# Performance work log

Measured on AMD Instinct MI355X. Metric: run time of the kernel, lower is better.

Reference implementation:

```python
import jax, jax.numpy as jnp
import numpy as np

B, C, H, W = 4, 256, 64, 64
E = C // 8  # embedding_channels = inChannels // k


def setup_inputs() -> dict:
    key = jax.random.key(0)
    ks = jax.random.split(key, 9)
    sc = 1.0 / np.sqrt(C)
    so = 1.0 / np.sqrt(E)
    return {
        "x": jax.random.normal(ks[0], (B, C, H, W), dtype=jnp.float32),
        "Wk": jax.random.normal(ks[1], (E, C), dtype=jnp.float32) * sc,
        "bk": jax.random.normal(ks[2], (E,), dtype=jnp.float32) * 0.01,
        "Wq": jax.random.normal(ks[3], (E, C), dtype=jnp.float32) * sc,
        "bq": jax.random.normal(ks[4], (E,), dtype=jnp.float32) * 0.01,
        "Wv": jax.random.normal(ks[5], (E, C), dtype=jnp.float32) * sc,
        "bv": jax.random.normal(ks[6], (E,), dtype=jnp.float32) * 0.01,
        "Wo": jax.random.normal(ks[7], (C, E), dtype=jnp.float32) * so,
        "bo": jax.random.normal(ks[8], (C,), dtype=jnp.float32) * 0.01,
    }


def reference(x, Wk, bk, Wq, bq, Wv, bv, Wo, bo):
    b, c, h, w = x.shape
    n = h * w
    gamma = jnp.float32(0.5)  # non-learned branch (learned=False default)

    def conv1x1(inp, Wt, bt):
        # 1x1 conv == channel-mixing matmul: [b,c,h,w] x [e,c] -> [b,e,h,w]
        return jnp.einsum('bchw,ec->behw', inp, Wt) + bt[None, :, None, None]

    f = conv1x1(x, Wk, bk).reshape(b, -1, n)  # key   [b,E,N]
    g = conv1x1(x, Wq, bq).reshape(b, -1, n)  # query [b,E,N]
    hx = conv1x1(x, Wv, bv).reshape(b, -1, n)  # value [b,E,N]

    s = jnp.einsum('bei,bej->bij', f, g)       # f^T @ g, [b,N,N]
    beta = jax.nn.softmax(s, axis=1)           # softmax over dim 1 (rows) as in torch
    v = jnp.einsum('bei,bij->bej', hx, beta)   # h @ beta, [b,E,N]
    v = v.reshape(b, -1, h, w)

    o = jnp.einsum('behw,ce->bchw', v, Wo) + bo[None, :, None, None]
    y = gamma * o + x
    return y, o, gamma
```

## Files before the change

kernel.cpp:

```cpp
#include <hip/hip_runtime.h>

#define B_ 4
#define C_ 256
#define N_ 4096
#define E_ 32

typedef _Float16 f16x8 __attribute__((ext_vector_type(8)));
typedef _Float16 f16x4 __attribute__((ext_vector_type(4)));
typedef _Float16 f16x2 __attribute__((ext_vector_type(2)));
typedef float f32x4 __attribute__((ext_vector_type(4)));

#define LOG2E 1.44269504088896f
#define EXP2(x) __builtin_amdgcn_exp2f(x)
#define PKRTZ(a, b) __builtin_bit_cast(f16x2, __builtin_amdgcn_cvt_pkrtz((a), (b)))

#define XSWZ(row, col) ((col) ^ ((((row) >> 2) & 7) << 3))

__global__ __launch_bounds__(256) void proj_kernel(
    const float* __restrict__ x,
    const float* __restrict__ Wk, const float* __restrict__ bk,
    const float* __restrict__ Wq, const float* __restrict__ bq,
    const float* __restrict__ Wv, const float* __restrict__ bv,
    const float* __restrict__ Wo,
    _Float16* __restrict__ Qb, _Float16* __restrict__ Kb, _Float16* __restrict__ Vt,
    _Float16* __restrict__ Wof16, float* __restrict__ out)
{
    const int b  = blockIdx.x >> 7;
    const int n0 = (blockIdx.x & 127) << 5;
    const int t    = threadIdx.x;
    const int lane = t & 63;
    const int wave = t >> 6;
    const int l15  = lane & 15;
    const int quad = lane >> 4;

    if (blockIdx.x < 256 && t < 8) {
        float4 wv = ((const float4*)(Wo + blockIdx.x * E_))[t];
        f16x4 tp = {(_Float16)wv.x, (_Float16)wv.y, (_Float16)wv.z, (_Float16)wv.w};
        *(f16x4*)&Wof16[blockIdx.x * E_ + t * 4] = tp;
    }
    if (blockIdx.x == 0 && t == 0)
        out[(size_t)2 * B_ * C_ * N_] = 0.5f;

    __shared__ _Float16 xT[32][264];
    __shared__ _Float16 Wl[32][264];
    __shared__ _Float16 vT[32][44];

    for (int i4 = t; i4 < (32 * 256) / 4; i4 += 256) {
        int j4 = (i4 & 7) * 4;
        int c  = i4 >> 3;
        float4 xv = *(const float4*)(x + (size_t)(b * C_ + c) * N_ + n0 + j4);
        xT[j4 + 0][XSWZ(j4 + 0, c)] = (_Float16)xv.x;
        xT[j4 + 1][XSWZ(j4 + 1, c)] = (_Float16)xv.y;
        xT[j4 + 2][XSWZ(j4 + 2, c)] = (_Float16)xv.z;
        xT[j4 + 3][XSWZ(j4 + 3, c)] = (_Float16)xv.w;
    }

    const float* Ws[3] = {Wk, Wq, Wv};
    const float* bs[3] = {bk, bq, bv};

    const int rowg = wave >> 1;
    const int et   = wave & 1;
    const int row  = rowg * 16 + l15;
    f16x8 Bf[8];

    for (int m = 0; m < 3; ++m) {
        for (int i4 = t; i4 < (E_ * C_) / 4; i4 += 256) {
            float4 wv = ((const float4*)Ws[m])[i4];
            int e = (i4 * 4) >> 8, c = (i4 * 4) & 255;
            f16x4 tp = {(_Float16)wv.x, (_Float16)wv.y, (_Float16)wv.z, (_Float16)wv.w};
            *(f16x4*)&Wl[e][XSWZ(e, c)] = tp;
        }
        __syncthreads();
        if (m == 0) {
            #pragma unroll
            for (int kk = 0; kk < 8; ++kk)
                Bf[kk] = *(const f16x8*)&xT[row][XSWZ(row, kk * 32 + quad * 8)];
        }
        const float sc = (m == 1) ? LOG2E : 1.0f;
        const float* bias = bs[m];
        f32x4 acc = {0.f, 0.f, 0.f, 0.f};
        #pragma unroll
        for (int kk = 0; kk < 8; ++kk) {
            const int e = et * 16 + l15;
            f16x8 Af = *(const f16x8*)&Wl[e][XSWZ(e, kk * 32 + quad * 8)];
            acc = __builtin_amdgcn_mfma_f32_16x16x32_f16(Af, Bf[kk], acc, 0, 0, 0);
        }
        const int n  = n0 + row;
        const int e0 = et * 16 + quad * 4;
        if (m == 2) {
            #pragma unroll
            for (int r = 0; r < 4; ++r)
                vT[e0 + r][row] = (_Float16)(acc[r] + bias[e0 + r]);
        } else {
            f16x4 st;
            #pragma unroll
            for (int r = 0; r < 4; ++r)
                st[r] = (_Float16)((acc[r] + bias[e0 + r]) * sc);
            _Float16* dst = (m == 0) ? Kb : Qb;
            *(f16x4*)&dst[(size_t)(b * N_ + n) * E_ + e0] = st;
        }
        __syncthreads();
    }

    if (t < 128) {
        const int e_s = t >> 2;
        const int nb  = t & 3;
        f16x8 v = *(const f16x8*)&vT[e_s][nb * 8];
        size_t base = ((size_t)(b * 128 + (n0 >> 5)) * 32 + e_s) * 32 + nb * 8;
        *(f16x8*)&Vt[base] = v;
    }
}

__global__ __launch_bounds__(512, 4) void attn_kernel(
    const _Float16* __restrict__ Qb, const _Float16* __restrict__ Kb,
    const _Float16* __restrict__ Vt, const _Float16* __restrict__ Wof16,
    const float* __restrict__ bo, const float* __restrict__ x,
    float* __restrict__ out)
{
    const int wave = threadIdx.x >> 6;
    const int lane = threadIdx.x & 63;
    const int l15  = lane & 15, quad = lane >> 4;
    const int jg   = blockIdx.x;
    const int b    = jg >> 7;
    const int j0   = (jg & 127) << 5;

    __shared__ __align__(16) char big[8][2][2304];
    __shared__ float    mls[8][2][2][16];
    __shared__ _Float16 Om[2][16][40];

    f16x8 Qf[2];
    #pragma unroll
    for (int cc = 0; cc < 2; ++cc)
        Qf[cc] = *(const f16x8*)(Qb + (size_t)(b * N_ + j0 + cc * 16 + l15) * E_ + quad * 8);

    f32x4 O0c[2], O1c[2];
    float mneg[2], lsum[2];
    #pragma unroll
    for (int cc = 0; cc < 2; ++cc) {
        O0c[cc] = (f32x4){0, 0, 0, 0}; O1c[cc] = (f32x4){0, 0, 0, 0};
        mneg[cc] = 0.f; lsum[cc] = 0.f;
    }

    const _Float16* Kp = Kb + (size_t)b * N_ * E_ + (size_t)(wave << 9) * E_;
    const _Float16* Vp = Vt + ((size_t)(b * 128 + wave * 16) << 10);

    f16x8 K0 = *(const f16x8*)(Kp + (size_t)(l15) * E_ + quad * 8);
    f16x8 K1 = *(const f16x8*)(Kp + (size_t)(16 + l15) * E_ + quad * 8);
    f16x8 K2 = *(const f16x8*)(Kp + (size_t)(32 + l15) * E_ + quad * 8);
    f16x8 K3 = *(const f16x8*)(Kp + (size_t)(48 + l15) * E_ + quad * 8);
    f16x8 Va0 = *(const f16x8*)(Vp + l15 * 32 + quad * 8);
    f16x8 Vc0 = *(const f16x8*)(Vp + (16 + l15) * 32 + quad * 8);
    f16x8 Va1 = *(const f16x8*)(Vp + 1024 + l15 * 32 + quad * 8);
    f16x8 Vc1 = *(const f16x8*)(Vp + 1024 + (16 + l15) * 32 + quad * 8);

    for (int it = 0; it < 8; ++it) {
        const int i0n = (it + 1) << 6;
        f32x4 S[2][4];
        {
            f32x4 c0 = {mneg[0], mneg[0], mneg[0], mneg[0]};
            f32x4 c1 = {mneg[1], mneg[1], mneg[1], mneg[1]};
            __builtin_amdgcn_s_setprio(1);
            S[0][0] = __builtin_amdgcn_mfma_f32_16x16x32_f16(K0, Qf[0], c0, 0, 0, 0);
            S[0][1] = __builtin_amdgcn_mfma_f32_16x16x32_f16(K1, Qf[0], c0, 0, 0, 0);
            S[0][2] = __builtin_amdgcn_mfma_f32_16x16x32_f16(K2, Qf[0], c0, 0, 0, 0);
            S[0][3] = __builtin_amdgcn_mfma_f32_16x16x32_f16(K3, Qf[0], c0, 0, 0, 0);
            S[1][0] = __builtin_amdgcn_mfma_f32_16x16x32_f16(K0, Qf[1], c1, 0, 0, 0);
            S[1][1] = __builtin_amdgcn_mfma_f32_16x16x32_f16(K1, Qf[1], c1, 0, 0, 0);
            S[1][2] = __builtin_amdgcn_mfma_f32_16x16x32_f16(K2, Qf[1], c1, 0, 0, 0);
            S[1][3] = __builtin_amdgcn_mfma_f32_16x16x32_f16(K3, Qf[1], c1, 0, 0, 0);
            __builtin_amdgcn_s_setprio(0);
        }
        K0 = *(const f16x8*)(Kp + (size_t)(i0n + l15) * E_ + quad * 8);
        K1 = *(const f16x8*)(Kp + (size_t)(i0n + 16 + l15) * E_ + quad * 8);
        K2 = *(const f16x8*)(Kp + (size_t)(i0n + 32 + l15) * E_ + quad * 8);
        K3 = *(const f16x8*)(Kp + (size_t)(i0n + 48 + l15) * E_ + quad * 8);

        #pragma unroll
        for (int cc = 0; cc < 2; ++cc) {
            float t0 = fmaxf(fmaxf(S[cc][0][0], S[cc][0][1]), S[cc][0][2]);
            float t1 = fmaxf(fmaxf(S[cc][0][3], S[cc][1][0]), S[cc][1][1]);
            float t2 = fmaxf(fmaxf(S[cc][1][2], S[cc][1][3]), S[cc][2][0]);
            float t3 = fmaxf(fmaxf(S[cc][2][1], S[cc][2][2]), S[cc][2][3]);
            float t4 = fmaxf(fmaxf(S[cc][3][0], S[cc][3][1]), S[cc][3][2]);
            float mxl = fmaxf(fmaxf(fmaxf(t0, t1), t2),
                              fmaxf(fmaxf(t3, t4), S[cc][3][3]));
            if (__any(mxl > 8.f)) {
                float mx = fmaxf(mxl, __shfl_xor(mxl, 16));
                mx = fmaxf(mx, __shfl_xor(mx, 32));
                float mc = fmaxf(mx, 0.f);
                float alpha = EXP2(-mc);
                mneg[cc] -= mc;
                lsum[cc] *= alpha;
                O0c[cc] *= alpha;
                O1c[cc] *= alpha;
                #pragma unroll
                for (int kt = 0; kt < 4; ++kt)
                    #pragma unroll
                    for (int r = 0; r < 4; ++r)
                        S[cc][kt][r] -= mc;
            }
            float p0  = EXP2(S[cc][0][0]), p1  = EXP2(S[cc][0][1]);
            float p2  = EXP2(S[cc][0][2]), p3  = EXP2(S[cc][0][3]);
            float p4  = EXP2(S[cc][1][0]), p5  = EXP2(S[cc][1][1]);
            float p6  = EXP2(S[cc][1][2]), p7  = EXP2(S[cc][1][3]);
            float p8  = EXP2(S[cc][2][0]), p9  = EXP2(S[cc][2][1]);
            float p10 = EXP2(S[cc][2][2]), p11 = EXP2(S[cc][2][3]);
            float p12 = EXP2(S[cc][3][0]), p13 = EXP2(S[cc][3][1]);
            float p14 = EXP2(S[cc][3][2]), p15 = EXP2(S[cc][3][3]);
            lsum[cc] += (((p0 + p1) + (p2 + p3)) + ((p4 + p5) + (p6 + p7)))
                      + (((p8 + p9) + (p10 + p11)) + ((p12 + p13) + (p14 + p15)));

            f16x2 a0 = PKRTZ(p0,  p1),  a1 = PKRTZ(p2,  p3);
            f16x2 a2 = PKRTZ(p4,  p5),  a3 = PKRTZ(p6,  p7);
            f16x2 a4 = PKRTZ(p8,  p9),  a5 = PKRTZ(p10, p11);
            f16x2 a6 = PKRTZ(p12, p13), a7 = PKRTZ(p14, p15);
            f16x4 wA0 = {a0[0], a0[1], a1[0], a1[1]};
            f16x4 wA1 = {a2[0], a2[1], a3[0], a3[1]};
            f16x4 wB0 = {a4[0], a4[1], a5[0], a5[1]};
            f16x4 wB1 = {a6[0], a6[1], a7[0], a7[1]};
            _Float16 (*pb)[72] = (_Float16 (*)[72])(big[wave][cc]);
            *(f16x4*)&pb[l15][quad * 4]      = wA0;
            *(f16x4*)&pb[l15][16 + quad * 4] = wA1;
            *(f16x4*)&pb[l15][32 + quad * 4] = wB0;
            *(f16x4*)&pb[l15][48 + quad * 4] = wB1;
        }
        f16x8 PA0, PB0, PA1, PB1;
        {
            _Float16 (*pb0)[72] = (_Float16 (*)[72])(big[wave][0]);
            _Float16 (*pb1)[72] = (_Float16 (*)[72])(big[wave][1]);
            PA0 = *(const f16x8*)&pb0[l15][quad * 8];
            PB0 = *(const f16x8*)&pb0[l15][32 + quad * 8];
            PA1 = *(const f16x8*)&pb1[l15][quad * 8];
            PB1 = *(const f16x8*)&pb1[l15][32 + quad * 8];
        }
        __builtin_amdgcn_s_setprio(1);
        O0c[0] = __builtin_amdgcn_mfma_f32_16x16x32_f16(Va0, PA0, O0c[0], 0, 0, 0);
        O1c[0] = __builtin_amdgcn_mfma_f32_16x16x32_f16(Vc0, PA0, O1c[0], 0, 0, 0);
        O0c[1] = __builtin_amdgcn_mfma_f32_16x16x32_f16(Va0, PA1, O0c[1], 0, 0, 0);
        O1c[1] = __builtin_amdgcn_mfma_f32_16x16x32_f16(Vc0, PA1, O1c[1], 0, 0, 0);
        O0c[0] = __builtin_amdgcn_mfma_f32_16x16x32_f16(Va1, PB0, O0c[0], 0, 0, 0);
        O1c[0] = __builtin_amdgcn_mfma_f32_16x16x32_f16(Vc1, PB0, O1c[0], 0, 0, 0);
        O0c[1] = __builtin_amdgcn_mfma_f32_16x16x32_f16(Va1, PB1, O0c[1], 0, 0, 0);
        O1c[1] = __builtin_amdgcn_mfma_f32_16x16x32_f16(Vc1, PB1, O1c[1], 0, 0, 0);
        __builtin_amdgcn_s_setprio(0);
        Va0 = *(const f16x8*)(Vp + (i0n << 5) + l15 * 32 + quad * 8);
        Vc0 = *(const f16x8*)(Vp + (i0n << 5) + (16 + l15) * 32 + quad * 8);
        Va1 = *(const f16x8*)(Vp + (i0n << 5) + 1024 + l15 * 32 + quad * 8);
        Vc1 = *(const f16x8*)(Vp + (i0n << 5) + 1024 + (16 + l15) * 32 + quad * 8);
    }

    #pragma unroll
    for (int cc = 0; cc < 2; ++cc) {
        float ls = lsum[cc];
        ls += __shfl_xor(ls, 16);
        ls += __shfl_xor(ls, 32);
        if (quad == 0) { mls[wave][0][cc][l15] = -mneg[cc]; mls[wave][1][cc][l15] = ls; }
    }
    __syncthreads();

    #pragma unroll
    for (int cc = 0; cc < 2; ++cc) {
        float M = -1e30f, ms[8], ls[8];
        #pragma unroll
        for (int s = 0; s < 8; ++s) {
            ms[s] = mls[s][0][cc][l15]; ls[s] = mls[s][1][cc][l15];
            M = fmaxf(M, ms[s]);
        }
        float L = 0.f;
        #pragma unroll
        for (int s = 0; s < 8; ++s) L += ls[s] * EXP2(ms[s] - M);
        const float w = EXP2(-mneg[cc] - M) / L;
        float (*osum)[34] = (float (*)[34])(big[wave][cc]);
        *(f32x4*)&osum[l15][quad * 4]      = O0c[cc] * w;
        *(f32x4*)&osum[l15][16 + quad * 4] = O1c[cc] * w;
    }
    __syncthreads();

    {
        const int j = threadIdx.x >> 5;
        const int e = threadIdx.x & 31;
        #pragma unroll
        for (int cc = 0; cc < 2; ++cc) {
            float a = 0.f;
            #pragma unroll
            for (int s = 0; s < 8; ++s)
                a += ((const float (*)[34])(big[s][cc]))[j][e];
            Om[cc][j][e] = (_Float16)a;
        }
    }
    __syncthreads();

    f16x8 Bf2[2];
    #pragma unroll
    for (int cc = 0; cc < 2; ++cc)
        Bf2[cc] = *(const f16x8*)&Om[cc][l15][quad * 8];
    float* out_y = out + (size_t)b * C_ * N_;
    float* out_o = out + (size_t)B_ * C_ * N_ + (size_t)b * C_ * N_;
    const float* xb = x + (size_t)b * C_ * N_;
    #pragma unroll
    for (int ct = 0; ct < 2; ++ct) {
        const int c0 = wave * 32 + ct * 16;
        f16x8 Af = *(const f16x8*)(Wof16 + (size_t)(c0 + l15) * E_ + quad * 8);
        f32x4 acc[2];
        f32x4 z = {0, 0, 0, 0};
        #pragma unroll
        for (int cc = 0; cc < 2; ++cc)
            acc[cc] = __builtin_amdgcn_mfma_f32_16x16x32_f16(Af, Bf2[cc], z, 0, 0, 0);
        #pragma unroll
        for (int r = 0; r < 4; ++r) {
            const int c = c0 + quad * 4 + r;
            #pragma unroll
            for (int cc = 0; cc < 2; ++cc) {
                size_t idx = (size_t)c * N_ + j0 + cc * 16 + l15;
                float ov = acc[cc][r] + bo[c];
                out_o[idx] = ov;
                out_y[idx] = 0.5f * ov + xb[idx];
            }
        }
    }
}

extern "C" void kernel_launch(void* const* d_in, const int* in_sizes, int n_in,
                              void* d_out, int out_size, void* d_ws, size_t ws_size,
                              hipStream_t stream)
{
    const float* x  = (const float*)d_in[0];
    const float* Wk = (const float*)d_in[1];
    const float* bk = (const float*)d_in[2];
    const float* Wq = (const float*)d_in[3];
    const float* bq = (const float*)d_in[4];
    const float* Wv = (const float*)d_in[5];
    const float* bv = (const float*)d_in[6];
    const float* Wo = (const float*)d_in[7];
    const float* bo = (const float*)d_in[8];
    float* out = (float*)d_out;

    char* ws = (char*)d_ws;
    _Float16* Qb    = (_Float16*)(ws);
    _Float16* Kb    = (_Float16*)(ws + (1u << 20));
    _Float16* Vt    = (_Float16*)(ws + (2u << 20));
    _Float16* Wof16 = (_Float16*)(ws + (3u << 20));

    proj_kernel<<<dim3(512), dim3(256), 0, stream>>>(
        x, Wk, bk, Wq, bq, Wv, bv, Wo, Qb, Kb, Vt, Wof16, out);
    attn_kernel<<<dim3(B_ * (N_ / 32)), dim3(512), 0, stream>>>(
        Qb, Kb, Vt, Wof16, bo, x, out);
}
```

Measured before the change: 121.2 us.

## Halve attention query tile to 16 columns and double grid size

Each attention block now handles 16 query columns instead of 32, so the grid doubles to 1024 blocks. Per-block shared memory and registers roughly halve, and launch bounds rise to 6 blocks per CU for more occupancy and better load balance. In exchange, every K and V tile is loaded by twice as many blocks, which doubles K/V traffic and the per-block reduction and epilogue overhead. Each wave also has fewer independent MFMAs between loads, leaving less to hide load latency.

```diff
diff --git a/kernel.cpp b/kernel.cpp
--- a/kernel.cpp
+++ b/kernel.cpp
@@ -111,7 +111,7 @@
     }
 }
 
-__global__ __launch_bounds__(512, 4) void attn_kernel(
+__global__ __launch_bounds__(512, 6) void attn_kernel(
     const _Float16* __restrict__ Qb, const _Float16* __restrict__ Kb,
     const _Float16* __restrict__ Vt, const _Float16* __restrict__ Wof16,
     const float* __restrict__ bo, const float* __restrict__ x,
@@ -121,25 +121,17 @@
     const int lane = threadIdx.x & 63;
     const int l15  = lane & 15, quad = lane >> 4;
     const int jg   = blockIdx.x;
-    const int b    = jg >> 7;
-    const int j0   = (jg & 127) << 5;
-
-    __shared__ __align__(16) char big[8][2][2304];
-    __shared__ float    mls[8][2][2][16];
-    __shared__ _Float16 Om[2][16][40];
-
-    f16x8 Qf[2];
-    #pragma unroll
-    for (int cc = 0; cc < 2; ++cc)
-        Qf[cc] = *(const f16x8*)(Qb + (size_t)(b * N_ + j0 + cc * 16 + l15) * E_ + quad * 8);
-
-    f32x4 O0c[2], O1c[2];
-    float mneg[2], lsum[2];
-    #pragma unroll
-    for (int cc = 0; cc < 2; ++cc) {
-        O0c[cc] = (f32x4){0, 0, 0, 0}; O1c[cc] = (f32x4){0, 0, 0, 0};
-        mneg[cc] = 0.f; lsum[cc] = 0.f;
-    }
+    const int b    = jg >> 8;
+    const int j0   = (jg & 255) << 4;
+
+    __shared__ __align__(16) char big[8][2304];
+    __shared__ float    mls[8][2][16];
+    __shared__ _Float16 Om[16][40];
+
+    f16x8 Qf = *(const f16x8*)(Qb + (size_t)(b * N_ + j0 + l15) * E_ + quad * 8);
+
+    f32x4 O0 = {0, 0, 0, 0}, O1 = {0, 0, 0, 0};
+    float mneg = 0.f, lsum = 0.f;
 
     const _Float16* Kp = Kb + (size_t)b * N_ * E_ + (size_t)(wave << 9) * E_;
     const _Float16* Vp = Vt + ((size_t)(b * 128 + wave * 16) << 10);
@@ -155,19 +147,14 @@
 
     for (int it = 0; it < 8; ++it) {
         const int i0n = (it + 1) << 6;
-        f32x4 S[2][4];
+        f32x4 S0, S1, S2, S3;
         {
-            f32x4 c0 = {mneg[0], mneg[0], mneg[0], mneg[0]};
-            f32x4 c1 = {mneg[1], mneg[1], mneg[1], mneg[1]};
+            f32x4 c0 = {mneg, mneg, mneg, mneg};
             __builtin_amdgcn_s_setprio(1);
-            S[0][0] = __builtin_amdgcn_mfma_f32_16x16x32_f16(K0, Qf[0], c0, 0, 0, 0);
-            S[0][1] = __builtin_amdgcn_mfma_f32_16x16x32_f16(K1, Qf[0], c0, 0, 0, 0);
-            S[0][2] = __builtin_amdgcn_mfma_f32_16x16x32_f16(K2, Qf[0], c0, 0, 0, 0);
-            S[0][3] = __builtin_amdgcn_mfma_f32_16x16x32_f16(K3, Qf[0], c0, 0, 0, 0);
-            S[1][0] = __builtin_amdgcn_mfma_f32_16x16x32_f16(K0, Qf[1], c1, 0, 0, 0);
-            S[1][1] = __builtin_amdgcn_mfma_f32_16x16x32_f16(K1, Qf[1], c1, 0, 0, 0);
-            S[1][2] = __builtin_amdgcn_mfma_f32_16x16x32_f16(K2, Qf[1], c1, 0, 0, 0);
-            S[1][3] = __builtin_amdgcn_mfma_f32_16x16x32_f16(K3, Qf[1], c1, 0, 0, 0);
+            S0 = __builtin_amdgcn_mfma_f32_16x16x32_f16(K0, Qf, c0, 0, 0, 0);
+            S1 = __builtin_amdgcn_mfma_f32_16x16x32_f16(K1, Qf, c0, 0, 0, 0);
+            S2 = __builtin_amdgcn_mfma_f32_16x16x32_f16(K2, Qf, c0, 0, 0, 0);
+            S3 = __builtin_amdgcn_mfma_f32_16x16x32_f16(K3, Qf, c0, 0, 0, 0);
             __builtin_amdgcn_s_setprio(0);
         }
         K0 = *(const f16x8*)(Kp + (size_t)(i0n + l15) * E_ + quad * 8);
@@ -175,40 +162,38 @@
         K2 = *(const f16x8*)(Kp + (size_t)(i0n + 32 + l15) * E_ + quad * 8);
         K3 = *(const f16x8*)(Kp + (size_t)(i0n + 48 + l15) * E_ + quad * 8);
 
-        #pragma unroll
-        for (int cc = 0; cc < 2; ++cc) {
-            float t0 = fmaxf(fmaxf(S[cc][0][0], S[cc][0][1]), S[cc][0][2]);
-            float t1 = fmaxf(fmaxf(S[cc][0][3], S[cc][1][0]), S[cc][1][1]);
-            float t2 = fmaxf(fmaxf(S[cc][1][2], S[cc][1][3]), S[cc][2][0]);
-            float t3 = fmaxf(fmaxf(S[cc][2][1], S[cc][2][2]), S[cc][2][3]);
-            float t4 = fmaxf(fmaxf(S[cc][3][0], S[cc][3][1]), S[cc][3][2]);
+        {
+            float t0 = fmaxf(fmaxf(S0[0], S0[1]), S0[2]);
+            float t1 = fmaxf(fmaxf(S0[3], S1[0]), S1[1]);
+            float t2 = fmaxf(fmaxf(S1[2], S1[3]), S2[0]);
+            float t3 = fmaxf(fmaxf(S2[1], S2[2]), S2[3]);
+            float t4 = fmaxf(fmaxf(S3[0], S3[1]), S3[2]);
             float mxl = fmaxf(fmaxf(fmaxf(t0, t1), t2),
-                              fmaxf(fmaxf(t3, t4), S[cc][3][3]));
+                              fmaxf(fmaxf(t3, t4), S3[3]));
             if (__any(mxl > 8.f)) {
                 float mx = fmaxf(mxl, __shfl_xor(mxl, 16));
                 mx = fmaxf(mx, __shfl_xor(mx, 32));
                 float mc = fmaxf(mx, 0.f);
                 float alpha = EXP2(-mc);
-                mneg[cc] -= mc;
-                lsum[cc] *= alpha;
-                O0c[cc] *= alpha;
-                O1c[cc] *= alpha;
+                mneg -= mc;
+                lsum *= alpha;
+                O0 *= alpha;
+                O1 *= alpha;
                 #pragma unroll
-                for (int kt = 0; kt < 4; ++kt)
-                    #pragma unroll
-                    for (int r = 0; r < 4; ++r)
-                        S[cc][kt][r] -= mc;
+                for (int r = 0; r < 4; ++r) {
+                    S0[r] -= mc; S1[r] -= mc; S2[r] -= mc; S3[r] -= mc;
+                }
             }
-            float p0  = EXP2(S[cc][0][0]), p1  = EXP2(S[cc][0][1]);
-            float p2  = EXP2(S[cc][0][2]), p3  = EXP2(S[cc][0][3]);
-            float p4  = EXP2(S[cc][1][0]), p5  = EXP2(S[cc][1][1]);
-            float p6  = EXP2(S[cc][1][2]), p7  = EXP2(S[cc][1][3]);
-            float p8  = EXP2(S[cc][2][0]), p9  = EXP2(S[cc][2][1]);
-            float p10 = EXP2(S[cc][2][2]), p11 = EXP2(S[cc][2][3]);
-            float p12 = EXP2(S[cc][3][0]), p13 = EXP2(S[cc][3][1]);
-            float p14 = EXP2(S[cc][3][2]), p15 = EXP2(S[cc][3][3]);
-            lsum[cc] += (((p0 + p1) + (p2 + p3)) + ((p4 + p5) + (p6 + p7)))
-                      + (((p8 + p9) + (p10 + p11)) + ((p12 + p13) + (p14 + p15)));
+            float p0  = EXP2(S0[0]), p1  = EXP2(S0[1]);
+            float p2  = EXP2(S0[2]), p3  = EXP2(S0[3]);
+            float p4  = EXP2(S1[0]), p5  = EXP2(S1[1]);
+            float p6  = EXP2(S1[2]), p7  = EXP2(S1[3]);
+            float p8  = EXP2(S2[0]), p9  = EXP2(S2[1]);
+            float p10 = EXP2(S2[2]), p11 = EXP2(S2[3]);
+            float p12 = EXP2(S3[0]), p13 = EXP2(S3[1]);
+            float p14 = EXP2(S3[2]), p15 = EXP2(S3[3]);
+            lsum += (((p0 + p1) + (p2 + p3)) + ((p4 + p5) + (p6 + p7)))
+                  + (((p8 + p9) + (p10 + p11)) + ((p12 + p13) + (p14 + p15)));
 
             f16x2 a0 = PKRTZ(p0,  p1),  a1 = PKRTZ(p2,  p3);
             f16x2 a2 = PKRTZ(p4,  p5),  a3 = PKRTZ(p6,  p7);
@@ -218,30 +203,23 @@
             f16x4 wA1 = {a2[0], a2[1], a3[0], a3[1]};
             f16x4 wB0 = {a4[0], a4[1], a5[0], a5[1]};
             f16x4 wB1 = {a6[0], a6[1], a7[0], a7[1]};
-            _Float16 (*pb)[72] = (_Float16 (*)[72])(big[wave][cc]);
+            _Float16 (*pb)[72] = (_Float16 (*)[72])(big[wave]);
             *(f16x4*)&pb[l15][quad * 4]      = wA0;
             *(f16x4*)&pb[l15][16 + quad * 4] = wA1;
             *(f16x4*)&pb[l15][32 + quad * 4] = wB0;
             *(f16x4*)&pb[l15][48 + quad * 4] = wB1;
         }
-        f16x8 PA0, PB0, PA1, PB1;
+        f16x8 PA, PB;
         {
-            _Float16 (*pb0)[72] = (_Float16 (*)[72])(big[wave][0]);
-            _Float16 (*pb1)[72] = (_Float16 (*)[72])(big[wave][1]);
-            PA0 = *(const f16x8*)&pb0[l15][quad * 8];
-            PB0 = *(const f16x8*)&pb0[l15][32 + quad * 8];
-            PA1 = *(const f16x8*)&pb1[l15][quad * 8];
-            PB1 = *(const f16x8*)&pb1[l15][32 + quad * 8];
+            _Float16 (*pb)[72] = (_Float16 (*)[72])(big[wave]);
+            PA = *(const f16x8*)&pb[l15][quad * 8];
+            PB = *(const f16x8*)&pb[l15][32 + quad * 8];
         }
         __builtin_amdgcn_s_setprio(1);
-        O0c[0] = __builtin_amdgcn_mfma_f32_16x16x32_f16(Va0, PA0, O0c[0], 0, 0, 0);
-        O1c[0] = __builtin_amdgcn_mfma_f32_16x16x32_f16(Vc0, PA0, O1c[0], 0, 0, 0);
-        O0c[1] = __builtin_amdgcn_mfma_f32_16x16x32_f16(Va0, PA1, O0c[1], 0, 0, 0);
-        O1c[1] = __builtin_amdgcn_mfma_f32_16x16x32_f16(Vc0, PA1, O1c[1], 0, 0, 0);
-        O0c[0] = __builtin_amdgcn_mfma_f32_16x16x32_f16(Va1, PB0, O0c[0], 0, 0, 0);
-        O1c[0] = __builtin_amdgcn_mfma_f32_16x16x32_f16(Vc1, PB0, O1c[0], 0, 0, 0);
-        O0c[1] = __builtin_amdgcn_mfma_f32_16x16x32_f16(Va1, PB1, O0c[1], 0, 0, 0);
-        O1c[1] = __builtin_amdgcn_mfma_f32_16x16x32_f16(Vc1, PB1, O1c[1], 0, 0, 0);
+        O0 = __builtin_amdgcn_mfma_f32_16x16x32_f16(Va0, PA, O0, 0, 0, 0);
+        O1 = __builtin_amdgcn_mfma_f32_16x16x32_f16(Vc0, PA, O1, 0, 0, 0);
+        O0 = __builtin_amdgcn_mfma_f32_16x16x32_f16(Va1, PB, O0, 0, 0, 0);
+        O1 = __builtin_amdgcn_mfma_f32_16x16x32_f16(Vc1, PB, O1, 0, 0, 0);
         __builtin_amdgcn_s_setprio(0);
         Va0 = *(const f16x8*)(Vp + (i0n << 5) + l15 * 32 + quad * 8);
         Vc0 = *(const f16x8*)(Vp + (i0n << 5) + (16 + l15) * 32 + quad * 8);
@@ -249,51 +227,43 @@
         Vc1 = *(const f16x8*)(Vp + (i0n << 5) + 1024 + (16 + l15) * 32 + quad * 8);
     }
 
-    #pragma unroll
-    for (int cc = 0; cc < 2; ++cc) {
-        float ls = lsum[cc];
+    {
+        float ls = lsum;
         ls += __shfl_xor(ls, 16);
         ls += __shfl_xor(ls, 32);
-        if (quad == 0) { mls[wave][0][cc][l15] = -mneg[cc]; mls[wave][1][cc][l15] = ls; }
+        if (quad == 0) { mls[wave][0][l15] = -mneg; mls[wave][1][l15] = ls; }
     }
     __syncthreads();
 
-    #pragma unroll
-    for (int cc = 0; cc < 2; ++cc) {
+    {
         float M = -1e30f, ms[8], ls[8];
         #pragma unroll
         for (int s = 0; s < 8; ++s) {
-            ms[s] = mls[s][0][cc][l15]; ls[s] = mls[s][1][cc][l15];
+            ms[s] = mls[s][0][l15]; ls[s] = mls[s][1][l15];
             M = fmaxf(M, ms[s]);
         }
         float L = 0.f;
         #pragma unroll
         for (int s = 0; s < 8; ++s) L += ls[s] * EXP2(ms[s] - M);
-        const float w = EXP2(-mneg[cc] - M) / L;
-        float (*osum)[34] = (float (*)[34])(big[wave][cc]);
-        *(f32x4*)&osum[l15][quad * 4]      = O0c[cc] * w;
-        *(f32x4*)&osum[l15][16 + quad * 4] = O1c[cc] * w;
+        const float w = EXP2(-mneg - M) / L;
+        float (*osum)[34] = (float (*)[34])(big[wave]);
+        *(f32x4*)&osum[l15][quad * 4]      = O0 * w;
+        *(f32x4*)&osum[l15][16 + quad * 4] = O1 * w;
     }
     __syncthreads();
 
     {
         const int j = threadIdx.x >> 5;
         const int e = threadIdx.x & 31;
-        #pragma unroll
-        for (int cc = 0; cc < 2; ++cc) {
-            float a = 0.f;
-            #pragma unroll
-            for (int s = 0; s < 8; ++s)
-                a += ((const float (*)[34])(big[s][cc]))[j][e];
-            Om[cc][j][e] = (_Float16)a;
-        }
+        float a = 0.f;
+        #pragma unroll
+        for (int s = 0; s < 8; ++s)
+            a += ((const float (*)[34])(big[s]))[j][e];
+        Om[j][e] = (_Float16)a;
     }
     __syncthreads();
 
-    f16x8 Bf2[2];
-    #pragma unroll
-    for (int cc = 0; cc < 2; ++cc)
-        Bf2[cc] = *(const f16x8*)&Om[cc][l15][quad * 8];
+    f16x8 Bf2 = *(const f16x8*)&Om[l15][quad * 8];
     float* out_y = out + (size_t)b * C_ * N_;
     float* out_o = out + (size_t)B_ * C_ * N_ + (size_t)b * C_ * N_;
     const float* xb = x + (size_t)b * C_ * N_;
@@ -301,21 +271,15 @@
     for (int ct = 0; ct < 2; ++ct) {
         const int c0 = wave * 32 + ct * 16;
         f16x8 Af = *(const f16x8*)(Wof16 + (size_t)(c0 + l15) * E_ + quad * 8);
-        f32x4 acc[2];
         f32x4 z = {0, 0, 0, 0};
-        #pragma unroll
-        for (int cc = 0; cc < 2; ++cc)
-            acc[cc] = __builtin_amdgcn_mfma_f32_16x16x32_f16(Af, Bf2[cc], z, 0, 0, 0);
+        f32x4 acc = __builtin_amdgcn_mfma_f32_16x16x32_f16(Af, Bf2, z, 0, 0, 0);
         #pragma unroll
         for (int r = 0; r < 4; ++r) {
             const int c = c0 + quad * 4 + r;
-            #pragma unroll
-            for (int cc = 0; cc < 2; ++cc) {
-                size_t idx = (size_t)c * N_ + j0 + cc * 16 + l15;
-                float ov = acc[cc][r] + bo[c];
-                out_o[idx] = ov;
-                out_y[idx] = 0.5f * ov + xb[idx];
-            }
+            size_t idx = (size_t)c * N_ + j0 + l15;
+            float ov = acc[r] + bo[c];
+            out_o[idx] = ov;
+            out_y[idx] = 0.5f * ov + xb[idx];
         }
     }
 }
@@ -343,6 +307,6 @@
 
     proj_kernel<<<dim3(512), dim3(256), 0, stream>>>(
         x, Wk, bk, Wq, bq, Wv, bv, Wo, Qb, Kb, Vt, Wof16, out);
-    attn_kernel<<<dim3(B_ * (N_ / 32)), dim3(512), 0, stream>>>(
+    attn_kernel<<<dim3(B_ * (N_ / 16)), dim3(512), 0, stream>>>(
         Qb, Kb, Vt, Wof16, bo, x, out);
 }
```

Result: slower. 189.1 us (+56.0%).
